# Kernel optimization log

Measured on AMD Instinct MI355X. Metric: run time of the kernel, lower is better.

## Reference

```python
import jax, jax.numpy as jnp
import numpy as np

B, D_IN, T = 8, 1024, 2048
CODEBOOK_SIZE, CODEBOOK_DIM = 8192, 8
EPS = 1e-12  # F.normalize default eps


def _l2_normalize(x, axis=-1):
    # matches torch F.normalize: x / max(||x||_2, eps)
    n = jnp.sqrt(jnp.sum(x * x, axis=axis, keepdims=True))
    return x / jnp.maximum(n, EPS)


def setup_inputs() -> dict:
    key = jax.random.key(0)
    k_z, k_wi, k_bi, k_wo, k_bo, k_cb = jax.random.split(key, 6)
    z = jax.random.normal(k_z, (B, D_IN, T), dtype=jnp.float32)
    # weight_norm(Conv1d) is a reparameterization; the effective weight is a
    # plain [out, in] matrix for a kernel_size=1 conv.
    w_in = jax.random.normal(k_wi, (CODEBOOK_DIM, D_IN), dtype=jnp.float32) * (1.0 / np.sqrt(D_IN))
    b_in = jax.random.normal(k_bi, (CODEBOOK_DIM,), dtype=jnp.float32) * 0.01
    w_out = jax.random.normal(k_wo, (D_IN, CODEBOOK_DIM), dtype=jnp.float32) * (1.0 / np.sqrt(CODEBOOK_DIM))
    b_out = jax.random.normal(k_bo, (D_IN,), dtype=jnp.float32) * 0.01
    codebook = jax.random.normal(k_cb, (CODEBOOK_SIZE, CODEBOOK_DIM), dtype=jnp.float32)
    return {"z": z, "w_in": w_in, "b_in": b_in, "w_out": w_out, "b_out": b_out, "codebook": codebook}


def reference(z, w_in, b_in, w_out, b_out, codebook):
    b, _, t = z.shape
    # in_project: 1x1 conv == matmul over channel dim
    z_e = jnp.einsum('od,bdt->bot', w_in, z) + b_in[None, :, None]  # [B, cd, T]

    # decode_latents
    enc = z_e.transpose(0, 2, 1).reshape(b * t, CODEBOOK_DIM)  # (b t) d
    enc_n = _l2_normalize(enc, axis=1)
    cb_n = _l2_normalize(codebook, axis=1)
    # dist = ||e||^2 - 2 e @ c^T + ||c||^2  (materializes [B*T, K] as original)
    dist = (jnp.sum(enc_n * enc_n, axis=1, keepdims=True)
            - 2.0 * (enc_n @ cb_n.T)
            + jnp.sum(cb_n * cb_n, axis=1)[None, :])
    indices = jnp.argmax(-dist, axis=1).reshape(b, t)  # [B, T] int
    # decode_code uses the UNnormalized codebook
    z_q = codebook[indices].transpose(0, 2, 1)  # [B, cd, T]

    # straight-through estimator
    z_q_st = z_e + jax.lax.stop_gradient(z_q - z_e)
    out = jnp.einsum('od,bdt->bot', w_out, z_q_st) + b_out[None, :, None]  # [B, D, T]

    commit_loss = jnp.zeros((b,), dtype=z.dtype)
    codebook_loss = jnp.zeros((b,), dtype=z.dtype)
    return (out, commit_loss, codebook_loss, indices, z_e)
```

## Files before the change

### kernel.cpp

```cpp
#include <hip/hip_runtime.h>
#include <math.h>

static constexpr int Bq  = 8;
static constexpr int DIN = 1024;
static constexpr int TTT = 2048;
static constexpr int KCB = 8192;

static constexpr int NCH = 64;
static constexpr int CPC = 128;

static constexpr size_t OUT_OFS  = 0;
static constexpr size_t LOSS_OFS = (size_t)Bq * DIN * TTT;
static constexpr size_t IDX_OFS  = LOSS_OFS + 16;
static constexpr size_t ZE_OFS   = IDX_OFS + (size_t)Bq * TTT;

static constexpr size_t WS_CBN  = 0;
static constexpr size_t WS_C2   = 65536;
static constexpr size_t WS_WT   = 73728;
static constexpr size_t WS_ENC  = 81920;
static constexpr size_t WS_Q    = 212992;
static constexpr size_t WS_PART = 344064;
static constexpr size_t WS_IDXI = WS_PART + (size_t)2 * NCH * 16384;

__global__ __launch_bounds__(256) void k0_prep(
    const float* __restrict__ w_in, const float* __restrict__ codebook,
    float* __restrict__ ws, float* __restrict__ out)
{
  int tid = blockIdx.x * 256 + threadIdx.x;
  if (tid < KCB) {
    const float4* cp = (const float4*)(codebook + (size_t)tid * 8);
    float4 a = cp[0], b = cp[1];
    float v[8] = {a.x, a.y, a.z, a.w, b.x, b.y, b.z, b.w};
    float n2 = 0.f;
#pragma unroll
    for (int o = 0; o < 8; o++) n2 = fmaf(v[o], v[o], n2);
    float dn = fmaxf(sqrtf(n2), 1e-12f);
    float u[8];
    float s2 = 0.f;
#pragma unroll
    for (int o = 0; o < 8; o++) { u[o] = v[o] / dn; s2 = fmaf(u[o], u[o], s2); }
    float4* wp = (float4*)(ws + WS_CBN + (size_t)tid * 8);
    wp[0] = make_float4(u[0], u[1], u[2], u[3]);
    wp[1] = make_float4(u[4], u[5], u[6], u[7]);
    ws[WS_C2 + tid] = 0.5f * s2;
  } else if (tid < KCB + DIN) {
    int d = tid - KCB;
#pragma unroll
    for (int o = 0; o < 8; o++) ws[WS_WT + (size_t)d * 8 + o] = w_in[(size_t)o * DIN + d];
  } else if (tid < KCB + DIN + 16) {
    out[LOSS_OFS + (tid - KCB - DIN)] = 0.f;
  }
}

__global__ __launch_bounds__(256, 2) void k1_proj_in(
    const float* __restrict__ z, const float* __restrict__ b_in,
    const float* __restrict__ wt, float* __restrict__ enc, float* __restrict__ out)
{
  __shared__ __align__(16) float lds[32 * 264 + 8 * 33];
  int tid = threadIdx.x;
  int b = blockIdx.x >> 6;
  int t0 = (blockIdx.x & 63) << 5;
  int dg = tid >> 3;
  int tt = tid & 7;
  const float* zb = z + (size_t)b * DIN * TTT + t0 + (tt << 2);
  const float4* wtp = (const float4*)wt;
  float4 acc[8];
#pragma unroll
  for (int o = 0; o < 8; o++) acc[o] = make_float4(0.f, 0.f, 0.f, 0.f);
#pragma unroll 4
  for (int i = 0; i < 32; i++) {
    int d = dg + (i << 5);
    float4 zv = *(const float4*)(zb + (size_t)d * TTT);
    float4 w0 = wtp[d * 2 + 0];
    float4 w1 = wtp[d * 2 + 1];
#define ACC1(o, wsc)                                    \
    acc[o].x = fmaf(wsc, zv.x, acc[o].x);               \
    acc[o].y = fmaf(wsc, zv.y, acc[o].y);               \
    acc[o].z = fmaf(wsc, zv.z, acc[o].z);               \
    acc[o].w = fmaf(wsc, zv.w, acc[o].w);
    ACC1(0, w0.x) ACC1(1, w0.y) ACC1(2, w0.z) ACC1(3, w0.w)
    ACC1(4, w1.x) ACC1(5, w1.y) ACC1(6, w1.z) ACC1(7, w1.w)
#undef ACC1
  }
  {
    float* pl = lds + dg * 264 + (tt << 2);
#pragma unroll
    for (int o = 0; o < 8; o++) *(float4*)(pl + (o << 5)) = acc[o];
  }
  __syncthreads();
  int o = tid >> 5;
  int t = tid & 31;
  float s = 0.f;
#pragma unroll
  for (int g = 0; g < 32; g++) s += lds[g * 264 + (o << 5) + t];
  s += b_in[o];
  out[ZE_OFS + ((size_t)b * 8 + o) * TTT + t0 + t] = s;
  float* nb = lds + 32 * 264;
  nb[o * 33 + t] = s;
  __syncthreads();
  float n2 = 0.f;
#pragma unroll
  for (int j = 0; j < 8; j++) { float v = nb[j * 33 + t]; n2 = fmaf(v, v, n2); }
  float dn = fmaxf(sqrtf(n2), 1e-12f);
  enc[((size_t)b * TTT + t0 + t) * 8 + o] = -(s / dn);
}

__global__ __launch_bounds__(256, 4) void k2_scan(
    const float* __restrict__ cbn, const float* __restrict__ c2h,
    const float* __restrict__ enc, float2* __restrict__ part)
{
  int tid = threadIdx.x;
  int rb = blockIdx.x >> 6;
  int ch = blockIdx.x & 63;
  int k0 = ch << 7;
  const float* cb = cbn + (size_t)k0 * 8;
  const float* hh = c2h + k0;
  int rbase = (rb << 10) + tid;

#define DECL_ROW(j) float4 m##j##a, m##j##b; float b##j = 3.4e38f; int i##j = 0;
  DECL_ROW(0) DECL_ROW(1) DECL_ROW(2) DECL_ROW(3)
#undef DECL_ROW
#define LOAD_ROW(j) {                                                         \
    const float4* ep = (const float4*)(enc + (size_t)(rbase + (j << 8)) * 8); \
    m##j##a = ep[0]; m##j##b = ep[1]; }
  LOAD_ROW(0) LOAD_ROW(1) LOAD_ROW(2) LOAD_ROW(3)
#undef LOAD_ROW

#pragma unroll 4
  for (int k = 0; k < CPC; k++) {
    float c0 = cb[k * 8 + 0], c1 = cb[k * 8 + 1];
    float c2 = cb[k * 8 + 2], c3 = cb[k * 8 + 3];
    float c4 = cb[k * 8 + 4], c5 = cb[k * 8 + 5];
    float c6 = cb[k * 8 + 6], c7 = cb[k * 8 + 7];
    float cc = hh[k];
    int kk = k0 + k;
#define STEP(j) {                                                             \
    float s = cc;                                                             \
    s = fmaf(m##j##a.x, c0, s); s = fmaf(m##j##a.y, c1, s);                   \
    s = fmaf(m##j##a.z, c2, s); s = fmaf(m##j##a.w, c3, s);                   \
    s = fmaf(m##j##b.x, c4, s); s = fmaf(m##j##b.y, c5, s);                   \
    s = fmaf(m##j##b.z, c6, s); s = fmaf(m##j##b.w, c7, s);                   \
    if (s < b##j) { b##j = s; i##j = kk; } }
    STEP(0) STEP(1) STEP(2) STEP(3)
#undef STEP
  }
#define STORE_ROW(j) \
  part[(size_t)ch * 16384 + rbase + (j << 8)] = make_float2(b##j, __int_as_float(i##j));
  STORE_ROW(0) STORE_ROW(1) STORE_ROW(2) STORE_ROW(3)
#undef STORE_ROW
}

__global__ __launch_bounds__(256) void k2b_reduce(
    const float* __restrict__ codebook, float* __restrict__ ws, float* __restrict__ out)
{
  int r = blockIdx.x * 256 + threadIdx.x;
  const float2* part = (const float2*)(ws + WS_PART);
  float best = 3.4e38f;
  int bi = 0;
#pragma unroll 8
  for (int ch = 0; ch < NCH; ch++) {
    float2 p = part[(size_t)ch * 16384 + r];
    if (p.x < best) { best = p.x; bi = __float_as_int(p.y); }
  }
  out[IDX_OFS + r] = (float)bi;
  ((int*)(ws + WS_IDXI))[r] = bi;
  const float4* cb = (const float4*)codebook;
  float4* q = (float4*)(ws + WS_Q + (size_t)r * 8);
  q[0] = cb[(size_t)bi * 2];
  q[1] = cb[(size_t)bi * 2 + 1];
}

__global__ __launch_bounds__(256) void k3_proj_out(
    const float* __restrict__ w_out, const float* __restrict__ b_out,
    const float* __restrict__ ws, float* __restrict__ out)
{
  int bx = blockIdx.x;
  int b = bx >> 7;
  int th = (bx >> 6) & 1;
  int dt = bx & 63;
  int tid = threadIdx.x;
  int t = (th << 10) + (tid << 2);
  const float4* qp = (const float4*)(ws + WS_Q + ((size_t)b * TTT + t) * 8);
  float4 c00 = qp[0], c01 = qp[1];
  float4 c10 = qp[2], c11 = qp[3];
  float4 c20 = qp[4], c21 = qp[5];
  float4 c30 = qp[6], c31 = qp[7];
  int d0 = dt << 4;
#pragma unroll 4
  for (int dd = 0; dd < 16; dd++) {
    int d = d0 + dd;
    const float* wr = w_out + (size_t)d * 8;
    float w0 = wr[0], w1 = wr[1], w2 = wr[2], w3 = wr[3];
    float w4 = wr[4], w5 = wr[5], w6 = wr[6], w7 = wr[7];
    float bb = b_out[d];
#define DOT8(lo, hi)                                                          \
    fmaf(w7, hi.w, fmaf(w6, hi.z, fmaf(w5, hi.y, fmaf(w4, hi.x,              \
    fmaf(w3, lo.w, fmaf(w2, lo.z, fmaf(w1, lo.y, fmaf(w0, lo.x, bb))))))))
    float4 r;
    r.x = DOT8(c00, c01);
    r.y = DOT8(c10, c11);
    r.z = DOT8(c20, c21);
    r.w = DOT8(c30, c31);
#undef DOT8
    *(float4*)(out + OUT_OFS + ((size_t)b * DIN + d) * TTT + t) = r;
  }
}

extern "C" void kernel_launch(void* const* d_in, const int* in_sizes, int n_in,
                              void* d_out, int out_size, void* d_ws, size_t ws_size,
                              hipStream_t stream) {
  const float* z        = (const float*)d_in[0];
  const float* w_in     = (const float*)d_in[1];
  const float* b_in     = (const float*)d_in[2];
  const float* w_out    = (const float*)d_in[3];
  const float* b_out    = (const float*)d_in[4];
  const float* codebook = (const float*)d_in[5];
  float* out = (float*)d_out;
  float* ws  = (float*)d_ws;

  k0_prep<<<dim3(37), dim3(256), 0, stream>>>(w_in, codebook, ws, out);
  k1_proj_in<<<dim3(512), dim3(256), 0, stream>>>(z, b_in, ws + WS_WT, ws + WS_ENC, out);
  k2_scan<<<dim3(1024), dim3(256), 0, stream>>>(ws + WS_CBN, ws + WS_C2, ws + WS_ENC,
                                                (float2*)(ws + WS_PART));
  k2b_reduce<<<dim3(64), dim3(256), 0, stream>>>(codebook, ws, out);
  k3_proj_out<<<dim3(1024), dim3(256), 0, stream>>>(w_out, b_out, ws, out);
}
```

Baseline: 196.3 us.

## Split input projection over channel halves and shrink scan row tiles

The input projection now splits the 1024-channel reduction into two halves across twice as many blocks, writing partial sums to workspace. A new combine kernel adds the halves plus bias, writes z_e, and normalizes the encodings. The codebook scan handles two rows per thread instead of four, doubling its grid and raising the occupancy hint. The aim is more parallelism and occupancy in the memory-bound projection and the scan, at the cost of an extra launch, an extra partial-sum round trip, and codebook loads amortized over fewer rows.

```diff
diff --git a/kernel.cpp b/kernel.cpp
--- a/kernel.cpp
+++ b/kernel.cpp
@@ -21,6 +21,7 @@
 static constexpr size_t WS_Q    = 212992;
 static constexpr size_t WS_PART = 344064;
 static constexpr size_t WS_IDXI = WS_PART + (size_t)2 * NCH * 16384;
+static constexpr size_t WS_P1   = WS_IDXI + 16384;
 
 __global__ __launch_bounds__(256) void k0_prep(
     const float* __restrict__ w_in, const float* __restrict__ codebook,
@@ -52,23 +53,25 @@
   }
 }
 
-__global__ __launch_bounds__(256, 2) void k1_proj_in(
-    const float* __restrict__ z, const float* __restrict__ b_in,
-    const float* __restrict__ wt, float* __restrict__ enc, float* __restrict__ out)
-{
-  __shared__ __align__(16) float lds[32 * 264 + 8 * 33];
+__global__ __launch_bounds__(256, 4) void k1_proj_in(
+    const float* __restrict__ z, const float* __restrict__ wt,
+    float* __restrict__ p1)
+{
+  __shared__ __align__(16) float lds[32 * 264];
   int tid = threadIdx.x;
-  int b = blockIdx.x >> 6;
-  int t0 = (blockIdx.x & 63) << 5;
+  int bx = blockIdx.x;
+  int b = bx >> 7;
+  int t0 = ((bx >> 1) & 63) << 5;
+  int dh = bx & 1;
   int dg = tid >> 3;
   int tt = tid & 7;
-  const float* zb = z + (size_t)b * DIN * TTT + t0 + (tt << 2);
-  const float4* wtp = (const float4*)wt;
+  const float* zb = z + (size_t)b * DIN * TTT + (size_t)(dh << 9) * TTT + t0 + (tt << 2);
+  const float4* wtp = (const float4*)(wt + (size_t)(dh << 9) * 8);
   float4 acc[8];
 #pragma unroll
   for (int o = 0; o < 8; o++) acc[o] = make_float4(0.f, 0.f, 0.f, 0.f);
-#pragma unroll 4
-  for (int i = 0; i < 32; i++) {
+#pragma unroll 8
+  for (int i = 0; i < 16; i++) {
     int d = dg + (i << 5);
     float4 zv = *(const float4*)(zb + (size_t)d * TTT);
     float4 w0 = wtp[d * 2 + 0];
@@ -93,38 +96,54 @@
   float s = 0.f;
 #pragma unroll
   for (int g = 0; g < 32; g++) s += lds[g * 264 + (o << 5) + t];
-  s += b_in[o];
-  out[ZE_OFS + ((size_t)b * 8 + o) * TTT + t0 + t] = s;
-  float* nb = lds + 32 * 264;
-  nb[o * 33 + t] = s;
-  __syncthreads();
+  p1[(((size_t)dh * 8 + b) * 8 + o) * TTT + t0 + t] = s;
+}
+
+__global__ __launch_bounds__(256) void k1c_combine(
+    const float* __restrict__ p1, const float* __restrict__ b_in,
+    float* __restrict__ enc, float* __restrict__ out)
+{
+  int r = blockIdx.x * 256 + threadIdx.x;
+  int b = r >> 11;
+  int t = r & 2047;
+  float v[8];
   float n2 = 0.f;
 #pragma unroll
-  for (int j = 0; j < 8; j++) { float v = nb[j * 33 + t]; n2 = fmaf(v, v, n2); }
+  for (int o = 0; o < 8; o++) {
+    float s = p1[(((size_t)b) * 8 + o) * TTT + t]
+            + p1[(((size_t)8 + b) * 8 + o) * TTT + t]
+            + b_in[o];
+    out[ZE_OFS + ((size_t)b * 8 + o) * TTT + t] = s;
+    v[o] = s;
+    n2 = fmaf(s, s, n2);
+  }
   float dn = fmaxf(sqrtf(n2), 1e-12f);
-  enc[((size_t)b * TTT + t0 + t) * 8 + o] = -(s / dn);
-}
-
-__global__ __launch_bounds__(256, 4) void k2_scan(
+  float4* ep = (float4*)(enc + (size_t)r * 8);
+  ep[0] = make_float4(-(v[0] / dn), -(v[1] / dn), -(v[2] / dn), -(v[3] / dn));
+  ep[1] = make_float4(-(v[4] / dn), -(v[5] / dn), -(v[6] / dn), -(v[7] / dn));
+}
+
+__global__ __launch_bounds__(256, 8) void k2_scan(
     const float* __restrict__ cbn, const float* __restrict__ c2h,
     const float* __restrict__ enc, float2* __restrict__ part)
 {
   int tid = threadIdx.x;
-  int rb = blockIdx.x >> 6;
-  int ch = blockIdx.x & 63;
+  int ch = blockIdx.x >> 5;
+  int rb = blockIdx.x & 31;
   int k0 = ch << 7;
   const float* cb = cbn + (size_t)k0 * 8;
   const float* hh = c2h + k0;
-  int rbase = (rb << 10) + tid;
-
-#define DECL_ROW(j) float4 m##j##a, m##j##b; float b##j = 3.4e38f; int i##j = 0;
-  DECL_ROW(0) DECL_ROW(1) DECL_ROW(2) DECL_ROW(3)
-#undef DECL_ROW
-#define LOAD_ROW(j) {                                                         \
-    const float4* ep = (const float4*)(enc + (size_t)(rbase + (j << 8)) * 8); \
-    m##j##a = ep[0]; m##j##b = ep[1]; }
-  LOAD_ROW(0) LOAD_ROW(1) LOAD_ROW(2) LOAD_ROW(3)
-#undef LOAD_ROW
+  int rbase = (rb << 9) + tid;
+
+  float4 m0a, m0b, m1a, m1b;
+  {
+    const float4* ep = (const float4*)(enc + (size_t)rbase * 8);
+    m0a = ep[0]; m0b = ep[1];
+    const float4* eq = (const float4*)(enc + (size_t)(rbase + 256) * 8);
+    m1a = eq[0]; m1b = eq[1];
+  }
+  float b0 = 3.4e38f, b1 = 3.4e38f;
+  int i0 = 0, i1 = 0;
 
 #pragma unroll 4
   for (int k = 0; k < CPC; k++) {
@@ -134,20 +153,25 @@
     float c6 = cb[k * 8 + 6], c7 = cb[k * 8 + 7];
     float cc = hh[k];
     int kk = k0 + k;
-#define STEP(j) {                                                             \
-    float s = cc;                                                             \
-    s = fmaf(m##j##a.x, c0, s); s = fmaf(m##j##a.y, c1, s);                   \
-    s = fmaf(m##j##a.z, c2, s); s = fmaf(m##j##a.w, c3, s);                   \
-    s = fmaf(m##j##b.x, c4, s); s = fmaf(m##j##b.y, c5, s);                   \
-    s = fmaf(m##j##b.z, c6, s); s = fmaf(m##j##b.w, c7, s);                   \
-    if (s < b##j) { b##j = s; i##j = kk; } }
-    STEP(0) STEP(1) STEP(2) STEP(3)
-#undef STEP
-  }
-#define STORE_ROW(j) \
-  part[(size_t)ch * 16384 + rbase + (j << 8)] = make_float2(b##j, __int_as_float(i##j));
-  STORE_ROW(0) STORE_ROW(1) STORE_ROW(2) STORE_ROW(3)
-#undef STORE_ROW
+    {
+      float s = cc;
+      s = fmaf(m0a.x, c0, s); s = fmaf(m0a.y, c1, s);
+      s = fmaf(m0a.z, c2, s); s = fmaf(m0a.w, c3, s);
+      s = fmaf(m0b.x, c4, s); s = fmaf(m0b.y, c5, s);
+      s = fmaf(m0b.z, c6, s); s = fmaf(m0b.w, c7, s);
+      if (s < b0) { b0 = s; i0 = kk; }
+    }
+    {
+      float s = cc;
+      s = fmaf(m1a.x, c0, s); s = fmaf(m1a.y, c1, s);
+      s = fmaf(m1a.z, c2, s); s = fmaf(m1a.w, c3, s);
+      s = fmaf(m1b.x, c4, s); s = fmaf(m1b.y, c5, s);
+      s = fmaf(m1b.z, c6, s); s = fmaf(m1b.w, c7, s);
+      if (s < b1) { b1 = s; i1 = kk; }
+    }
+  }
+  part[(size_t)ch * 16384 + rbase]       = make_float2(b0, __int_as_float(i0));
+  part[(size_t)ch * 16384 + rbase + 256] = make_float2(b1, __int_as_float(i1));
 }
 
 __global__ __launch_bounds__(256) void k2b_reduce(
@@ -219,8 +243,9 @@
   float* ws  = (float*)d_ws;
 
   k0_prep<<<dim3(37), dim3(256), 0, stream>>>(w_in, codebook, ws, out);
-  k1_proj_in<<<dim3(512), dim3(256), 0, stream>>>(z, b_in, ws + WS_WT, ws + WS_ENC, out);
-  k2_scan<<<dim3(1024), dim3(256), 0, stream>>>(ws + WS_CBN, ws + WS_C2, ws + WS_ENC,
+  k1_proj_in<<<dim3(1024), dim3(256), 0, stream>>>(z, ws + WS_WT, ws + WS_P1);
+  k1c_combine<<<dim3(64), dim3(256), 0, stream>>>(ws + WS_P1, b_in, ws + WS_ENC, out);
+  k2_scan<<<dim3(2048), dim3(256), 0, stream>>>(ws + WS_CBN, ws + WS_C2, ws + WS_ENC,
                                                 (float2*)(ws + WS_PART));
   k2b_reduce<<<dim3(64), dim3(256), 0, stream>>>(codebook, ws, out);
   k3_proj_out<<<dim3(1024), dim3(256), 0, stream>>>(w_out, b_out, ws, out);
```

Result: slower. 204.7 us (+4.2%).
